# Kernel tuning notes

Measured on AMD Instinct MI355X. Metric: run time of the kernel, lower is better.

## Reference

```python
import jax, jax.numpy as jnp
import numpy as np

B, S, H, NH = 2, 2048, 1024, 16
HD = H // NH


def setup_inputs() -> dict:
    key = jax.random.key(0)
    ks = jax.random.split(key, 14)
    lim = 1.0 / np.sqrt(H)  # torch Linear default init range
    def lin(ka, kb):
        W = jax.random.uniform(ka, (H, H), jnp.float32, -lim, lim)
        b = jax.random.uniform(kb, (H,), jnp.float32, -lim, lim)
        return W, b
    Wq, bq = lin(ks[0], ks[1])
    Wk, bk = lin(ks[2], ks[3])
    Wv, bv = lin(ks[4], ks[5])
    Wo, bo = lin(ks[6], ks[7])
    return {
        "query": jax.random.normal(ks[8], (B, S, H), jnp.float32),
        "key": jax.random.normal(ks[9], (B, S, H), jnp.float32),
        "value": jax.random.normal(ks[10], (B, S, H), jnp.float32),
        "attn_mask": jax.random.randint(ks[11], (B, S, S), 0, 2).astype(bool),
        "relative_time": jax.random.normal(ks[12], (B, 1, S, S), jnp.float32),
        "Wq": Wq, "bq": bq, "Wk": Wk, "bk": bk,
        "Wv": Wv, "bv": bv, "Wo": Wo, "bo": bo,
    }


def reference(query, key, value, attn_mask, relative_time,
              Wq, bq, Wk, bk, Wv, bv, Wo, bo):
    Bq, Sq, _ = query.shape
    Skv = key.shape[1]
    # projections (torch Linear: x @ W^T + b)
    Q = (query @ Wq.T + bq).reshape(Bq, Sq, NH, HD).transpose(0, 2, 1, 3)
    K = (key @ Wk.T + bk).reshape(Bq, Skv, NH, HD).transpose(0, 2, 1, 3)
    V = (value @ Wv.T + bv).reshape(Bq, Skv, NH, HD).transpose(0, 2, 1, 3)
    scale = HD ** (-0.5)
    # NOTE: bias added BEFORE scaling, matching the original (non-standard)
    scores = jnp.einsum("bhqd,bhkd->bhqk", Q, K)
    scores = (scores + relative_time) * scale
    scores = jnp.where(attn_mask[:, None, :, :], scores, -jnp.inf)
    attn = jax.nn.softmax(scores.astype(jnp.float32), axis=-1).astype(scores.dtype)
    attn = jnp.nan_to_num(attn, nan=0.0)
    # dropout is identity in eval mode (dropout_rate applied only when training)
    out = jnp.einsum("bhqk,bhkd->bhqd", attn, V)
    out = out.transpose(0, 2, 1, 3).reshape(Bq, Sq, H)
    return out @ Wo.T + bo
```

## Files before the change

kernel.cpp:

```cpp
#include <hip/hip_runtime.h>
#include <hip/hip_bf16.h>

constexpr int BATCH = 2, SEQ = 2048, HDIM = 1024, NHEADS = 16, HEADD = 64;
constexpr int MROWS = BATCH * SEQ;
constexpr float QSCALE = 0.18033688011112042f;

typedef short short8  __attribute__((ext_vector_type(8)));
typedef float f32x4   __attribute__((ext_vector_type(4)));
typedef float f32x16  __attribute__((ext_vector_type(16)));
typedef int   int4v   __attribute__((ext_vector_type(4)));
typedef unsigned short ushort4v __attribute__((ext_vector_type(4)));

static __device__ __forceinline__ short f2bf(float f) {
    __hip_bfloat16 h = __float2bfloat16(f);
    return *reinterpret_cast<short*>(&h);
}

static __device__ __forceinline__ int cvt_pk_bf16(float a, float b) {
    int r;
    asm("v_cvt_pk_bf16_f32 %0, %1, %2" : "=v"(r) : "v"(a), "v"(b));
    return r;
}

static __device__ __forceinline__ float bfbits2f(unsigned short u) {
    return __builtin_bit_cast(float, (unsigned int)u << 16);
}

static __device__ __forceinline__ void gload_lds16(const void* g, void* l) {
    __builtin_amdgcn_global_load_lds(
        (const __attribute__((address_space(1))) unsigned int*)g,
        (__attribute__((address_space(3))) unsigned int*)l, 16, 0, 0);
}

__global__ void cvt_all_kernel(const float* __restrict__ q, const float* __restrict__ k,
                               const float* __restrict__ v, const float* __restrict__ w0,
                               const float* __restrict__ w1, const float* __restrict__ w2,
                               const float* __restrict__ w3,
                               short* __restrict__ xq, short* __restrict__ xk,
                               short* __restrict__ xv, short* __restrict__ o0,
                               short* __restrict__ o1, short* __restrict__ o2,
                               short* __restrict__ o3, int n4x, int n4w) {
    int i = blockIdx.x * blockDim.x + threadIdx.x;
    const int stride = gridDim.x * blockDim.x;
    const int total = 3 * n4x + 4 * n4w;
    for (; i < total; i += stride) {
        const float* in; short* out; int j = i;
        if (j < 3 * n4x) {
            if (j >= 2 * n4x)      { in = v; out = xv; j -= 2 * n4x; }
            else if (j >= n4x)     { in = k; out = xk; j -= n4x; }
            else                   { in = q; out = xq; }
        } else {
            j -= 3 * n4x;
            if (j >= 3 * n4w)      { in = w3; out = o3; j -= 3 * n4w; }
            else if (j >= 2 * n4w) { in = w2; out = o2; j -= 2 * n4w; }
            else if (j >= n4w)     { in = w1; out = o1; j -= n4w; }
            else                   { in = w0; out = o0; }
        }
        const float4 val = reinterpret_cast<const float4*>(in)[j];
        short4 o;
        o.x = f2bf(val.x); o.y = f2bf(val.y); o.z = f2bf(val.z); o.w = f2bf(val.w);
        reinterpret_cast<short4*>(out)[j] = o;
    }
}

__global__ void detect_mask_kernel(const unsigned int* __restrict__ m, int* flag) {
    const int tid = threadIdx.x;
    int gt1 = 0, isf = 0;
    for (int i = 0; i < 4; ++i) {
        unsigned int wv = m[tid + 256 * i];
        if (wv > 1u) gt1 = 1;
        if (wv == 0x3F800000u) isf = 1;
    }
    __shared__ int s_gt1, s_isf;
    if (tid == 0) { s_gt1 = 0; s_isf = 0; }
    __syncthreads();
    if (gt1) atomicOr(&s_gt1, 1);
    if (isf) atomicOr(&s_isf, 1);
    __syncthreads();
    if (tid == 0) flag[0] = s_gt1 ? (s_isf ? 2 : 1) : 0;
}

__global__ void fuse_rel_kernel(const float* __restrict__ rel, const void* __restrict__ mask,
                                const int* __restrict__ flag, short* __restrict__ rT,
                                int nThr) {
    const int f = flag[0];
    int i = blockIdx.x * blockDim.x + threadIdx.x;
    const int stride = gridDim.x * blockDim.x;
    for (; i < nThr; i += stride) {
        const int q    = i & 2047;
        const int kv16 = (i >> 11) & 127;
        const int b    = i >> 18;
        const long base = ((long)(b * 2048 + q)) * 2048 + kv16 * 16;
        float4 rv[4];
        #pragma unroll
        for (int g = 0; g < 4; ++g)
            rv[g] = *reinterpret_cast<const float4*>(rel + base + 4 * g);
        bool mk[16];
        if (f == 1) {
            const unsigned int* mp = (const unsigned int*)((const unsigned char*)mask + base);
            #pragma unroll
            for (int wd = 0; wd < 4; ++wd) {
                const unsigned int mw = mp[wd];
                #pragma unroll
                for (int s = 0; s < 4; ++s) mk[wd * 4 + s] = ((mw >> (8 * s)) & 0xffu) != 0;
            }
        } else if (f == 0) {
            const int* mp = (const int*)mask + base;
            #pragma unroll
            for (int j = 0; j < 16; ++j) mk[j] = mp[j] != 0;
        } else {
            const float* mp = (const float*)mask + base;
            #pragma unroll
            for (int j = 0; j < 16; ++j) mk[j] = mp[j] != 0.0f;
        }
        const float* rp = reinterpret_cast<const float*>(&rv[0]);
        #pragma unroll
        for (int g = 0; g < 4; ++g) {
            short4 o;
            short* op = reinterpret_cast<short*>(&o);
            #pragma unroll
            for (int j = 0; j < 4; ++j) {
                const int idx = 4 * g + j;
                op[j] = f2bf(mk[idx] ? rp[idx] * QSCALE : -1e30f);
            }
            *reinterpret_cast<short4*>(rT + (((long)(b * 512 + kv16 * 4 + g)) * 2048 + q) * 4) = o;
        }
    }
}

template<typename EPI>
static __device__ __forceinline__
void gemm_core(const short* A, const short* Bw, int K, int m0, int n0, EPI epi) {
    __shared__ short As[128 * 64];
    __shared__ short Bs[128 * 64];
    const int tid  = threadIdx.x;
    const int lane = tid & 63;
    const int w    = tid >> 6;
    const int lo   = lane & 15, hi = lane >> 4;
    const int wm   = w >> 1, wn = w & 1;

    f32x4 acc[4][4] = {};

    const int arow = tid >> 3;
    const int acol = (tid & 7) * 8;
    const long aBase = (long)(m0 + arow) * K + acol;
    const long bBase = (long)(n0 + arow) * K + acol;

    for (int k0 = 0; k0 < K; k0 += 64) {
        for (int i = 0; i < 4; ++i) {
            gload_lds16(A  + aBase + (long)i * 32 * K + k0, (char*)As + i * 4096 + tid * 16);
            gload_lds16(Bw + bBase + (long)i * 32 * K + k0, (char*)Bs + i * 4096 + tid * 16);
        }
        __syncthreads();
        for (int ks = 0; ks < 2; ++ks) {
            short8 af[4], bf[4];
            const int koff = ks * 32 + hi * 8;
            for (int fm = 0; fm < 4; ++fm)
                af[fm] = *reinterpret_cast<const short8*>(&As[(wm * 64 + fm * 16 + lo) * 64 + koff]);
            for (int fn = 0; fn < 4; ++fn)
                bf[fn] = *reinterpret_cast<const short8*>(&Bs[(wn * 64 + fn * 16 + lo) * 64 + koff]);
            for (int fm = 0; fm < 4; ++fm)
                for (int fn = 0; fn < 4; ++fn)
                    acc[fm][fn] = __builtin_amdgcn_mfma_f32_16x16x32_bf16(
                        af[fm], bf[fn], acc[fm][fn], 0, 0, 0);
        }
        __syncthreads();
    }

    for (int fm = 0; fm < 4; ++fm)
        for (int fn = 0; fn < 4; ++fn) {
            const int n = n0 + wn * 64 + fn * 16 + lo;
            const int mB = m0 + wm * 64 + fm * 16 + hi * 4;
            for (int r = 0; r < 4; ++r) epi(mB + r, n, acc[fm][fn][r]);
        }
}

__global__ __launch_bounds__(256, 2)
void qkv_gemm(const short* xq, const short* xk, const short* xv,
              const short* wq, const short* wk, const short* wv,
              const float* bq, const float* bk, const float* bv,
              short* Qb, short* Kb, short* Vt) {
    const int which = blockIdx.x >> 8;
    const int bid   = blockIdx.x & 255;
    const int m0 = (bid >> 3) << 7;
    const int n0 = (bid & 7) << 7;
    const short* A    = which == 0 ? xq : which == 1 ? xk : xv;
    const short* W    = which == 0 ? wq : which == 1 ? wk : wv;
    const float* bias = which == 0 ? bq : which == 1 ? bk : bv;
    short* C          = which == 0 ? Qb : which == 1 ? Kb : Vt;
    const float scale = which == 0 ? QSCALE : 1.0f;
    gemm_core(A, W, HDIM, m0, n0, [&](int m, int n, float v) {
        v = (v + bias[n]) * scale;
        const int b = m >> 11, s = m & (SEQ - 1);
        const int h = n >> 6, d = n & 63;
        long idx;
        if (which != 2) idx = (((long)(b * NHEADS + h)) * SEQ + s) * HEADD + d;
        else            idx = (((long)(b * NHEADS + h)) * HEADD + d) * SEQ + s;
        C[idx] = f2bf(v);
    });
}

__global__ __launch_bounds__(256, 2)
void out_gemm(const short* A, const short* W, const float* bias, float* Cout) {
    const int bid = blockIdx.x;
    const int m0 = (bid >> 3) << 7;
    const int n0 = (bid & 7) << 7;
    gemm_core(A, W, HDIM, m0, n0, [&](int m, int n, float v) {
        Cout[(long)m * HDIM + n] = v + bias[n];
    });
}

__global__ __launch_bounds__(256, 4)
void attn_fwd(const short* __restrict__ Qb, const short* __restrict__ Kb,
              const short* __restrict__ Vtb, const short* __restrict__ rT,
              short* __restrict__ Ob) {
    __shared__ short Ks[2][64 * 64];
    __shared__ short Vs[2][64 * 64];
    const int tid  = threadIdx.x;
    const int lane = tid & 63;
    const int wv   = tid >> 6;
    const int qp   = wv & 1;
    const int t    = wv >> 1;
    const int l31  = lane & 31, hi2 = lane >> 5;
    const int wg = ((blockIdx.x & 7) << 7) + (blockIdx.x >> 3);
    const int qt = wg & 31, h = (wg >> 5) & 15, b = wg >> 9;
    const int bh = b * NHEADS + h;
    const int q0 = qt * 64 + qp * 32 + l31;

    short8 qf[4];
    {
        const short* qp_ = Qb + ((long)bh * SEQ + q0) * HEADD + hi2 * 8;
        #pragma unroll
        for (int s = 0; s < 4; ++s)
            qf[s] = *reinterpret_cast<const short8*>(qp_ + s * 16);
    }

    float lsum = 0.0f;
    f32x16 oacc0 = {}, oacc1 = {};

    const int srow  = tid >> 3;
    const int scolb = (tid & 7) * 16;
    const int scolK = scolb ^ ((srow & 7) << 4);
    const char* KbB = (const char*)Kb + ((long)bh * SEQ + srow) * 128 + scolK;
    const char* VbB = (const char*)Vtb + ((long)bh * HEADD + srow) * ((long)SEQ * 2) + scolK;

    auto stage = [&](int buf, int kt) {
        #pragma unroll
        for (int i = 0; i < 2; ++i) {
            gload_lds16(KbB + ((long)kt * 64 + i * 32) * 128,
                        (char*)&Ks[buf][0] + i * 4096 + tid * 16);
            gload_lds16(VbB + (long)i * 32 * (SEQ * 2) + (long)kt * 128,
                        (char*)&Vs[buf][0] + i * 4096 + tid * 16);
        }
    };

    ushort4v rbuf[4];
    auto loadRel = [&](int kt) {
        #pragma unroll
        for (int g = 0; g < 4; ++g) {
            const int p4 = kt * 16 + t * 8 + 2 * g + hi2;
            rbuf[g] = *reinterpret_cast<const ushort4v*>(
                rT + (((long)(b * 512 + p4)) * 2048 + q0) * 4);
        }
    };

    stage(0, 0);
    loadRel(0);
    __syncthreads();

    const int rsw = (l31 & 7) << 4;

    for (int kt = 0; kt < SEQ / 64; ++kt) {
        const int cb = kt & 1;
        if (kt < SEQ / 64 - 1) stage(cb ^ 1, kt + 1);

        f32x16 sc;
        #pragma unroll
        for (int g = 0; g < 4; ++g)
            #pragma unroll
            for (int j = 0; j < 4; ++j)
                sc[4 * g + j] = bfbits2f(rbuf[g][j]);
        loadRel(kt < SEQ / 64 - 1 ? kt + 1 : 0);

        const char* kls = (const char*)&Ks[cb][0];
        const char* kr  = kls + (t * 32 + l31) * 128;
        __builtin_amdgcn_s_setprio(1);
        #pragma unroll
        for (int s = 0; s < 4; ++s) {
            short8 kf = *reinterpret_cast<const short8*>(kr + ((s * 32 + hi2 * 16) ^ rsw));
            sc = __builtin_amdgcn_mfma_f32_32x32x16_bf16(kf, qf[s], sc, 0, 0, 0);
        }
        __builtin_amdgcn_s_setprio(0);

        int X[8];
        #pragma unroll
        for (int i2 = 0; i2 < 8; ++i2) {
            const float p0 = __builtin_amdgcn_exp2f(sc[2 * i2]);
            const float p1 = __builtin_amdgcn_exp2f(sc[2 * i2 + 1]);
            lsum += p0 + p1;
            X[i2] = cvt_pk_bf16(p0, p1);
        }
        int pa[2][4];
        #pragma unroll
        for (int u = 0; u < 2; ++u) {
            auto r0 = __builtin_amdgcn_permlane32_swap(X[4 * u + 0], X[4 * u + 2], false, false);
            auto r1 = __builtin_amdgcn_permlane32_swap(X[4 * u + 1], X[4 * u + 3], false, false);
            pa[u][0] = (int)r0[0];
            pa[u][1] = (int)r1[0];
            pa[u][2] = (int)r0[1];
            pa[u][3] = (int)r1[1];
        }

        const char* vls = (const char*)&Vs[cb][0];
        __builtin_amdgcn_s_setprio(1);
        #pragma unroll
        for (int dt = 0; dt < 2; ++dt) {
            const char* vr = vls + (dt * 32 + l31) * 128;
            #pragma unroll
            for (int u = 0; u < 2; ++u) {
                const int s = 2 * t + u;
                short8 vf = *reinterpret_cast<const short8*>(vr + ((s * 32 + hi2 * 16) ^ rsw));
                int4v pw = { pa[u][0], pa[u][1], pa[u][2], pa[u][3] };
                if (dt == 0)
                    oacc0 = __builtin_amdgcn_mfma_f32_32x32x16_bf16(
                        __builtin_bit_cast(short8, pw), vf, oacc0, 0, 0, 0);
                else
                    oacc1 = __builtin_amdgcn_mfma_f32_32x32x16_bf16(
                        __builtin_bit_cast(short8, pw), vf, oacc1, 0, 0, 0);
            }
        }
        __builtin_amdgcn_s_setprio(0);
        __syncthreads();
    }

    lsum += __shfl_xor(lsum, 32, 64);

    float* cmbO = (float*)&Ks[0][0];
    float* cmbL = (float*)&Vs[0][0];
    if (t == 1) {
        #pragma unroll
        for (int r = 0; r < 16; ++r) {
            const int qloc = (r & 3) + 8 * (r >> 2) + 4 * hi2;
            cmbO[(qp * 32 + qloc) * 64 + l31]      = oacc0[r];
            cmbO[(qp * 32 + qloc) * 64 + 32 + l31] = oacc1[r];
        }
        if (hi2 == 0) cmbL[qp * 32 + l31] = lsum;
    }
    __syncthreads();
    if (t == 0) {
        const float ltot = lsum + cmbL[qp * 32 + l31];
        const float inv  = ltot > 0.0f ? 1.0f / ltot : 0.0f;
        #pragma unroll
        for (int r = 0; r < 16; ++r) {
            const int qloc = (r & 3) + 8 * (r >> 2) + 4 * hi2;
            const float invr = __shfl(inv, qloc, 64);
            const int qg = qt * 64 + qp * 32 + qloc;
            const long obase = ((long)b * SEQ + qg) * HDIM + h * 64 + l31;
            const float o0 = oacc0[r] + cmbO[(qp * 32 + qloc) * 64 + l31];
            const float o1 = oacc1[r] + cmbO[(qp * 32 + qloc) * 64 + 32 + l31];
            Ob[obase]      = f2bf(o0 * invr);
            Ob[obase + 32] = f2bf(o1 * invr);
        }
    }
}

extern "C" void kernel_launch(void* const* d_in, const int* in_sizes, int n_in,
                              void* d_out, int out_size, void* d_ws, size_t ws_size,
                              hipStream_t stream) {
    const float* q    = (const float*)d_in[0];
    const float* k    = (const float*)d_in[1];
    const float* v    = (const float*)d_in[2];
    const void*  mask = d_in[3];
    const float* rel  = (const float*)d_in[4];
    const float* Wq   = (const float*)d_in[5];
    const float* bq   = (const float*)d_in[6];
    const float* Wk   = (const float*)d_in[7];
    const float* bk   = (const float*)d_in[8];
    const float* Wv   = (const float*)d_in[9];
    const float* bv   = (const float*)d_in[10];
    const float* Wo   = (const float*)d_in[11];
    const float* bo   = (const float*)d_in[12];
    (void)in_sizes; (void)n_in; (void)out_size; (void)ws_size;

    char* ws = (char*)d_ws;
    size_t off = 0;
    auto alloc = [&](size_t bytes) {
        char* p = ws + off;
        off += (bytes + 255) & ~(size_t)255;
        return p;
    };
    const size_t xBytes = (size_t)MROWS * HDIM * 2;
    const size_t wBytes = (size_t)HDIM * HDIM * 2;
    const size_t poolBytes = 3 * xBytes + 3 * wBytes;

    short* Qb  = (short*)alloc(xBytes);
    short* Kb  = (short*)alloc(xBytes);
    short* Vt  = (short*)alloc(xBytes);
    short* wob = (short*)alloc(wBytes);
    int*   flag = (int*)alloc(256);
    char* pool = (char*)alloc(poolBytes);
    short* Ab  = (short*)alloc(xBytes);

    short* xq  = (short*)(pool);
    short* xk  = (short*)(pool + xBytes);
    short* xv  = (short*)(pool + 2 * xBytes);
    short* wqb = (short*)(pool + 3 * xBytes);
    short* wkb = (short*)(pool + 3 * xBytes + wBytes);
    short* wvb = (short*)(pool + 3 * xBytes + 2 * wBytes);
    short* rT  = (short*)(pool);

    const int n4x = MROWS * HDIM / 4, n4w = HDIM * HDIM / 4;
    cvt_all_kernel<<<2048, 256, 0, stream>>>(q, k, v, Wq, Wk, Wv, Wo,
                                             xq, xk, xv, wqb, wkb, wvb, wob, n4x, n4w);
    detect_mask_kernel<<<1, 256, 0, stream>>>((const unsigned int*)mask, flag);

    qkv_gemm<<<768, 256, 0, stream>>>(xq, xk, xv, wqb, wkb, wvb,
                                      bq, bk, bv, Qb, Kb, Vt);

    const int relThr = BATCH * 128 * 2048;
    fuse_rel_kernel<<<2048, 256, 0, stream>>>(rel, mask, flag, rT, relThr);

    attn_fwd<<<1024, 256, 0, stream>>>(Qb, Kb, Vt, rT, Ab);

    out_gemm<<<256, 256, 0, stream>>>(Ab, wob, bo, (float*)d_out);
}
```

Baseline: 169.3 us.

## Use 128x64 output GEMM tiles, refine attention LDS swizzle and waitcnt pipelining

The output projection GEMM moves to 128x64 tiles and launches 512 blocks instead of 256, to fill more compute units on the device. In the attention kernel, the LDS XOR swizzle now also mixes in row bits 3-4 to cut bank conflicts. The full __syncthreads calls become explicit s_waitcnt vmcnt plus s_barrier, so the next K/V stage and rel loads can stay in flight while the current tile is computed. The hand-counted vmcnt values must match the real number of outstanding loads, or correctness breaks.

```diff
diff --git a/kernel.cpp b/kernel.cpp
--- a/kernel.cpp
+++ b/kernel.cpp
@@ -128,18 +128,19 @@
     }
 }
 
-template<typename EPI>
+template<int BN, typename EPI>
 static __device__ __forceinline__
 void gemm_core(const short* A, const short* Bw, int K, int m0, int n0, EPI epi) {
+    constexpr int NFRAG = BN / 32;
     __shared__ short As[128 * 64];
-    __shared__ short Bs[128 * 64];
+    __shared__ short Bs[BN * 64];
     const int tid  = threadIdx.x;
     const int lane = tid & 63;
     const int w    = tid >> 6;
     const int lo   = lane & 15, hi = lane >> 4;
     const int wm   = w >> 1, wn = w & 1;
 
-    f32x4 acc[4][4] = {};
+    f32x4 acc[4][NFRAG] = {};
 
     const int arow = tid >> 3;
     const int acol = (tid & 7) * 8;
@@ -147,29 +148,38 @@
     const long bBase = (long)(n0 + arow) * K + acol;
 
     for (int k0 = 0; k0 < K; k0 += 64) {
-        for (int i = 0; i < 4; ++i) {
-            gload_lds16(A  + aBase + (long)i * 32 * K + k0, (char*)As + i * 4096 + tid * 16);
+        #pragma unroll
+        for (int i = 0; i < 4; ++i)
+            gload_lds16(A + aBase + (long)i * 32 * K + k0, (char*)As + i * 4096 + tid * 16);
+        #pragma unroll
+        for (int i = 0; i < NFRAG; ++i)
             gload_lds16(Bw + bBase + (long)i * 32 * K + k0, (char*)Bs + i * 4096 + tid * 16);
-        }
         __syncthreads();
+        #pragma unroll
         for (int ks = 0; ks < 2; ++ks) {
-            short8 af[4], bf[4];
+            short8 af[4], bf[NFRAG];
             const int koff = ks * 32 + hi * 8;
+            #pragma unroll
             for (int fm = 0; fm < 4; ++fm)
                 af[fm] = *reinterpret_cast<const short8*>(&As[(wm * 64 + fm * 16 + lo) * 64 + koff]);
-            for (int fn = 0; fn < 4; ++fn)
-                bf[fn] = *reinterpret_cast<const short8*>(&Bs[(wn * 64 + fn * 16 + lo) * 64 + koff]);
+            #pragma unroll
+            for (int fn = 0; fn < NFRAG; ++fn)
+                bf[fn] = *reinterpret_cast<const short8*>(&Bs[(wn * (BN / 2) + fn * 16 + lo) * 64 + koff]);
+            #pragma unroll
             for (int fm = 0; fm < 4; ++fm)
-                for (int fn = 0; fn < 4; ++fn)
+                #pragma unroll
+                for (int fn = 0; fn < NFRAG; ++fn)
                     acc[fm][fn] = __builtin_amdgcn_mfma_f32_16x16x32_bf16(
                         af[fm], bf[fn], acc[fm][fn], 0, 0, 0);
         }
         __syncthreads();
     }
 
+    #pragma unroll
     for (int fm = 0; fm < 4; ++fm)
-        for (int fn = 0; fn < 4; ++fn) {
-            const int n = n0 + wn * 64 + fn * 16 + lo;
+        #pragma unroll
+        for (int fn = 0; fn < NFRAG; ++fn) {
+            const int n = n0 + wn * (BN / 2) + fn * 16 + lo;
             const int mB = m0 + wm * 64 + fm * 16 + hi * 4;
             for (int r = 0; r < 4; ++r) epi(mB + r, n, acc[fm][fn][r]);
         }
@@ -189,7 +199,7 @@
     const float* bias = which == 0 ? bq : which == 1 ? bk : bv;
     short* C          = which == 0 ? Qb : which == 1 ? Kb : Vt;
     const float scale = which == 0 ? QSCALE : 1.0f;
-    gemm_core(A, W, HDIM, m0, n0, [&](int m, int n, float v) {
+    gemm_core<128>(A, W, HDIM, m0, n0, [&](int m, int n, float v) {
         v = (v + bias[n]) * scale;
         const int b = m >> 11, s = m & (SEQ - 1);
         const int h = n >> 6, d = n & 63;
@@ -203,9 +213,9 @@
 __global__ __launch_bounds__(256, 2)
 void out_gemm(const short* A, const short* W, const float* bias, float* Cout) {
     const int bid = blockIdx.x;
-    const int m0 = (bid >> 3) << 7;
-    const int n0 = (bid & 7) << 7;
-    gemm_core(A, W, HDIM, m0, n0, [&](int m, int n, float v) {
+    const int m0 = (bid >> 4) << 7;
+    const int n0 = (bid & 15) << 6;
+    gemm_core<64>(A, W, HDIM, m0, n0, [&](int m, int n, float v) {
         Cout[(long)m * HDIM + n] = v + bias[n];
     });
 }
@@ -240,7 +250,7 @@
 
     const int srow  = tid >> 3;
     const int scolb = (tid & 7) * 16;
-    const int scolK = scolb ^ ((srow & 7) << 4);
+    const int scolK = scolb ^ ((((srow & 7) ^ ((srow >> 3) & 3))) << 4);
     const char* KbB = (const char*)Kb + ((long)bh * SEQ + srow) * 128 + scolK;
     const char* VbB = (const char*)Vtb + ((long)bh * HEADD + srow) * ((long)SEQ * 2) + scolK;
 
@@ -266,13 +276,18 @@
 
     stage(0, 0);
     loadRel(0);
-    __syncthreads();
-
-    const int rsw = (l31 & 7) << 4;
-
-    for (int kt = 0; kt < SEQ / 64; ++kt) {
+
+    const int rsw = (((l31 & 7) ^ ((l31 >> 3) & 3))) << 4;
+    const int NT = SEQ / 64;
+
+    for (int kt = 0; kt < NT; ++kt) {
         const int cb = kt & 1;
-        if (kt < SEQ / 64 - 1) stage(cb ^ 1, kt + 1);
+        const bool hasNext = (kt < NT - 1);
+        if (hasNext) stage(cb ^ 1, kt + 1);
+        if (hasNext) asm volatile("s_waitcnt vmcnt(8)" ::: "memory");
+        else         asm volatile("s_waitcnt vmcnt(4)" ::: "memory");
+        __builtin_amdgcn_s_barrier();
+        asm volatile("" ::: "memory");
 
         f32x16 sc;
         #pragma unroll
@@ -280,7 +295,7 @@
             #pragma unroll
             for (int j = 0; j < 4; ++j)
                 sc[4 * g + j] = bfbits2f(rbuf[g][j]);
-        loadRel(kt < SEQ / 64 - 1 ? kt + 1 : 0);
+        if (hasNext) loadRel(kt + 1);
 
         const char* kls = (const char*)&Ks[cb][0];
         const char* kr  = kls + (t * 32 + l31) * 128;
@@ -330,7 +345,9 @@
             }
         }
         __builtin_amdgcn_s_setprio(0);
-        __syncthreads();
+
+        asm volatile("" ::: "memory");
+        __builtin_amdgcn_s_barrier();
     }
 
     lsum += __shfl_xor(lsum, 32, 64);
@@ -422,5 +439,5 @@
 
     attn_fwd<<<1024, 256, 0, stream>>>(Qb, Kb, Vt, rT, Ab);
 
-    out_gemm<<<256, 256, 0, stream>>>(Ab, wob, bo, (float*)d_out);
-}
+    out_gemm<<<512, 256, 0, stream>>>(Ab, wob, bo, (float*)d_out);
+}
```

Result: faster. 162.7 us (-3.9%).
